# Kernel tuning notes

Hardware: AMD Instinct MI355X
Metric: run time of the kernel (lower is better)

The kernel has to match this reference:

```python
import jax, jax.numpy as jnp
import numpy as np

B, N, D = 4, 8192, 512
L, W, S = 64, 64, 32  # num_tokens, win_size, stride


def setup_inputs() -> dict:
    key = jax.random.key(0)
    ks = jax.random.split(key, 12)
    inp = {
        "feats": jax.random.normal(ks[0], (B, N, D), jnp.float32),
        "coords": jax.random.normal(ks[1], (B, N, 2), jnp.float32) * 100.0,
        "mask": jnp.zeros((B, N), dtype=bool),
        "z": jax.random.normal(ks[2], (L, D), jnp.float32) * 0.02,
        "Wq": jax.random.normal(ks[3], (D, D), jnp.float32) * 0.01,
        "Wk": jax.random.normal(ks[4], (D, D), jnp.float32) * 0.01,
        "Wv": jax.random.normal(ks[5], (D, D), jnp.float32) * 0.01,
        "W1": jax.random.normal(ks[6], (D, 2), jnp.float32) * 0.05,
        "b1": jnp.zeros((D,), jnp.float32),
        "W2": jax.random.normal(ks[7], (D, D), jnp.float32) * 0.01,
        "b2": jnp.zeros((D,), jnp.float32),
        "Wo": jax.random.normal(ks[8], (D, D), jnp.float32) * 0.01,
        "bo": jnp.zeros((D,), jnp.float32),
    }
    return inp


def reference(feats, coords, mask, z, Wq, Wk, Wv, W1, b1, W2, b2, Wo, bo):
    # mask is all-False: every token valid, N_valid == N, segments are
    # contiguous blocks of P = N // L tokens (seg_id = floor(i*L/N)).
    Bz, Nn, Dd = feats.shape
    Ll = z.shape[0]
    P = Nn // Ll  # tokens per segment

    # LayerNorm over feature dim (no affine, eps=1e-5 as in F.layer_norm)
    mu = feats.mean(-1, keepdims=True)
    var = feats.var(-1, keepdims=True)
    f_ln = (feats - mu) * jax.lax.rsqrt(var + 1e-5)

    # per-sample coordinate normalization (torch std is unbiased, ddof=1)
    c_mu = coords.mean(1, keepdims=True)
    c_sd = coords.std(1, keepdims=True, ddof=1) + 1e-8
    c_n = (coords - c_mu) / c_sd

    f_seg = f_ln.reshape(Bz, Ll, P, Dd)
    c_seg = c_n.reshape(Bz, Ll, P, 2)

    # static sliding windows within each segment (last window may be partial)
    starts = np.arange(0, P, S)                      # [nw]
    idx = starts[:, None] + np.arange(W)[None, :]    # [nw, W]
    valid = jnp.asarray(idx < P)                     # [nw, W] bool
    idx_c = np.minimum(idx, P - 1)
    cnt = valid.sum(-1).astype(feats.dtype)          # [nw]

    f_win = f_seg[:, :, idx_c]                       # [B,L,nw,W,D]
    c_win = c_seg[:, :, idx_c]                       # [B,L,nw,W,2]

    vmask = valid.astype(feats.dtype)[None, None, :, :, None]
    c_mean = (c_win * vmask).sum(3) / cnt[None, None, :, None]   # [B,L,nw,2]
    pos_in = c_win - c_mean[:, :, :, None, :]
    h = jax.nn.relu(jnp.einsum('blnwc,dc->blnwd', pos_in, W1) + b1)
    pos_bias = jnp.einsum('blnwd,ed->blnwe', h, W2) + b2

    q = z @ Wq.T                                     # [L,D]
    k = jnp.einsum('blnwd,ed->blnwe', f_win, Wk) + pos_bias
    v = jnp.einsum('blnwd,ed->blnwe', f_win, Wv)

    temperature = jnp.sqrt(jnp.asarray(Dd, feats.dtype))
    logits = jnp.einsum('ld,blnwd->blnw', q, k) / temperature
    logits = jnp.clip(logits, -10.0, 10.0)
    logits = jnp.where(valid[None, None], logits, -jnp.inf)
    attn = jax.nn.softmax(logits, axis=-1)           # [B,L,nw,W]

    z_win = jnp.einsum('blnw,blnwd->blnd', attn, v)  # [B,L,nw,D]
    z_l = z_win.mean(2)                              # average over windows
    return z_l @ Wo.T + bo                           # [B,L,D]
```

## Files before the change

kernel.cpp:

```cpp
#include <hip/hip_runtime.h>

#define Bz 4
#define Nn 8192
#define Dd 512
#define Ll 64
#define Pp 128
#define Ww 64
#define Ss 32
#define NW 4

__global__ __launch_bounds__(256) void pre1(
    const float* __restrict__ coords, const float* __restrict__ b2,
    const float* __restrict__ Wq, const float* __restrict__ Wk,
    const float* __restrict__ W2,
    const float* __restrict__ Wv, const float* __restrict__ Wo,
    float* __restrict__ cstats,
    float* __restrict__ M1, float* __restrict__ M2,
    float* __restrict__ WvoT, float* __restrict__ vb8) {
    __shared__ float As[64][65];
    __shared__ float Bs[64][36];
    __shared__ float b2s[64];
    __shared__ double dred[16];
    int bid = blockIdx.x, tid = threadIdx.x;
    int wv = tid >> 6, lane = tid & 63;

    if (bid < 384) {
        int role = bid >> 7;
        int wb = bid & 127;
        int m0 = (wb >> 4) * 64;
        int n0 = (wb & 15) * 32;
        const float* Amat = (role == 2) ? Wv : Wq;
        const float* Bmat = (role == 0) ? Wk : (role == 1) ? W2 : Wo;
        float* Cmat = (role == 0) ? M1 : (role == 1) ? M2 : WvoT;
        int tx = tid & 31, ty = tid >> 5;
        float acc[8] = {0.f, 0.f, 0.f, 0.f, 0.f, 0.f, 0.f, 0.f};
        for (int k0 = 0; k0 < Dd; k0 += 64) {
            int r = tid >> 4, c4 = (tid & 15) * 4;
#pragma unroll
            for (int i = 0; i < 4; ++i) {
                int kk = r + 16 * i;
                float4 v = *(const float4*)&Amat[(size_t)(k0 + kk) * Dd + m0 + c4];
                As[c4 + 0][kk] = v.x; As[c4 + 1][kk] = v.y;
                As[c4 + 2][kk] = v.z; As[c4 + 3][kk] = v.w;
            }
            if (role == 2) {
#pragma unroll
                for (int i = 0; i < 2; ++i) {
                    int nn = r + 16 * i;
                    float4 v = *(const float4*)&Bmat[(size_t)(n0 + nn) * Dd + k0 + c4];
                    Bs[c4 + 0][nn] = v.x; Bs[c4 + 1][nn] = v.y;
                    Bs[c4 + 2][nn] = v.z; Bs[c4 + 3][nn] = v.w;
                }
            } else {
                int kr = tid >> 3, c8 = (tid & 7) * 4;
#pragma unroll
                for (int i = 0; i < 2; ++i) {
                    int kk = kr + 32 * i;
                    float4 v = *(const float4*)&Bmat[(size_t)(k0 + kk) * Dd + n0 + c8];
                    *(float4*)&Bs[kk][c8] = v;
                }
            }
            __syncthreads();
#pragma unroll 16
            for (int kk = 0; kk < 64; ++kk) {
                float bv = Bs[kk][tx];
#pragma unroll
                for (int i = 0; i < 8; ++i)
                    acc[i] = fmaf(As[ty + 8 * i][kk], bv, acc[i]);
            }
            __syncthreads();
        }
#pragma unroll
        for (int i = 0; i < 8; ++i)
            Cmat[(size_t)(m0 + ty + 8 * i) * Dd + n0 + tx] = acc[i];
    } else if (bid < 392) {
        int j = bid - 384;
        if (tid < 64) b2s[tid] = b2[j * 64 + tid];
        __syncthreads();
        float a0 = 0.f, a1 = 0.f;
#pragma unroll 4
        for (int ee = 0; ee < 64; ++ee) {
            int e = j * 64 + ee;
            float be = b2s[ee];
            a0 = fmaf(be, Wq[(size_t)e * Dd + tid], a0);
            a1 = fmaf(be, Wq[(size_t)e * Dd + tid + 256], a1);
        }
        vb8[j * Dd + tid] = a0;
        vb8[j * Dd + tid + 256] = a1;
    } else {
        int b = bid - 392;
        double sx = 0, sy = 0, sxx = 0, syy = 0;
        const float4* cp = (const float4*)(coords + (size_t)b * Nn * 2);
        for (int i = tid; i < Nn / 2; i += 256) {
            float4 v = cp[i];
            sx  += (double)v.x + (double)v.z;
            sy  += (double)v.y + (double)v.w;
            sxx += (double)v.x * v.x + (double)v.z * v.z;
            syy += (double)v.y * v.y + (double)v.w * v.w;
        }
        for (int o = 32; o > 0; o >>= 1) {
            sx  += __shfl_down(sx,  o); sy  += __shfl_down(sy,  o);
            sxx += __shfl_down(sxx, o); syy += __shfl_down(syy, o);
        }
        if (lane == 0) {
            dred[wv * 4 + 0] = sx;  dred[wv * 4 + 1] = sy;
            dred[wv * 4 + 2] = sxx; dred[wv * 4 + 3] = syy;
        }
        __syncthreads();
        if (tid == 0) {
            double tx = 0, ty = 0, txx = 0, tyy = 0;
            for (int i = 0; i < 4; ++i) {
                tx += dred[i * 4 + 0]; ty += dred[i * 4 + 1];
                txx += dred[i * 4 + 2]; tyy += dred[i * 4 + 3];
            }
            const double N = (double)Nn;
            double mux = tx / N, muy = ty / N;
            double vx = (txx - N * mux * mux) / (N - 1.0);
            double vy = (tyy - N * muy * muy) / (N - 1.0);
            cstats[b * 4 + 0] = (float)mux;
            cstats[b * 4 + 1] = (float)muy;
            cstats[b * 4 + 2] = (float)sqrt(vx) + 1e-8f;
            cstats[b * 4 + 3] = (float)sqrt(vy) + 1e-8f;
        }
    }
}

__global__ __launch_bounds__(256) void qkg_k(
    const float* __restrict__ z, const float* __restrict__ M1,
    const float* __restrict__ M2, const float* __restrict__ vb8,
    float* __restrict__ QK, float* __restrict__ G,
    float* __restrict__ sqk4, float* __restrict__ qb2) {
    __shared__ float zs[Dd];
    __shared__ float pq[8][128];
    __shared__ float pg[8][128];
    __shared__ float red[8];
    int bid = blockIdx.x, tid = threadIdx.x;
    int l = bid & 63, ch = bid >> 6;
    int wv = tid >> 6, lane = tid & 63;

    zs[tid]       = z[(size_t)l * Dd + tid];
    zs[tid + 256] = z[(size_t)l * Dd + tid + 256];
    __syncthreads();

    if (ch == 0) {
        float vba = 0.f, vbb = 0.f;
#pragma unroll
        for (int j = 0; j < 8; ++j) {
            vba += vb8[j * Dd + tid];
            vbb += vb8[j * Dd + tid + 256];
        }
        float p = zs[tid] * vba + zs[tid + 256] * vbb;
        for (int o = 32; o > 0; o >>= 1) p += __shfl_xor(p, o);
        if (lane == 0) red[4 + wv] = p;
    }

    {
        int qd = tid & 31, h = tid >> 5;
        int cb = ch * 128 + qd * 4;
        float4 aq = make_float4(0.f, 0.f, 0.f, 0.f);
        float4 ag = make_float4(0.f, 0.f, 0.f, 0.f);
        for (int d = h * 64; d < h * 64 + 64; ++d) {
            float zd = zs[d];
            float4 m1 = *(const float4*)&M1[(size_t)d * Dd + cb];
            float4 m2 = *(const float4*)&M2[(size_t)d * Dd + cb];
            aq.x = fmaf(zd, m1.x, aq.x); aq.y = fmaf(zd, m1.y, aq.y);
            aq.z = fmaf(zd, m1.z, aq.z); aq.w = fmaf(zd, m1.w, aq.w);
            ag.x = fmaf(zd, m2.x, ag.x); ag.y = fmaf(zd, m2.y, ag.y);
            ag.z = fmaf(zd, m2.z, ag.z); ag.w = fmaf(zd, m2.w, ag.w);
        }
        *(float4*)&pq[h][qd * 4] = aq;
        *(float4*)&pg[h][qd * 4] = ag;
    }
    __syncthreads();
    if (tid < 128) {
        float vq = 0.f, vg = 0.f;
#pragma unroll
        for (int hh = 0; hh < 8; ++hh) { vq += pq[hh][tid]; vg += pg[hh][tid]; }
        QK[(size_t)l * Dd + ch * 128 + tid] = vq;
        G [(size_t)l * Dd + ch * 128 + tid] = vg;
        float s = vq;
        for (int o = 32; o > 0; o >>= 1) s += __shfl_xor(s, o);
        if (lane == 0) red[wv] = s;
    }
    __syncthreads();
    if (tid == 0) sqk4[ch * 64 + l] = red[0] + red[1];
    if (ch == 0 && tid == 32) qb2[l] = red[4] + red[5] + red[6] + red[7];
}

__global__ __launch_bounds__(512) void attn2(
    const float* __restrict__ feats, const float* __restrict__ coords,
    const float* __restrict__ cstats,
    const float* __restrict__ QKm, const float* __restrict__ Gm,
    const float* __restrict__ sqk4, const float* __restrict__ qb2,
    const float* __restrict__ W1, const float* __restrict__ b1,
    const float* __restrict__ WvoT, const float* __restrict__ bo,
    float* __restrict__ out) {
    __shared__ float  qk_s[Dd];
    __shared__ float4 wpack[Dd];
    __shared__ float  scx[Pp], scy[Pp];
    __shared__ float  smu[Pp], srs[Pp], sa[Pp];
    __shared__ float  shs[NW * Ww];
    __shared__ float  sar[NW][Ww];
    __shared__ float  swt[Pp];
    __shared__ float  scm[8];
    __shared__ float  s2red[NW];
    __shared__ float  soff;
    __shared__ float  red8[8][Dd];
    __shared__ float  fm_s[Dd];

    int bx = blockIdx.x;
    int l = bx & 63, b = bx >> 6;
    int tid = threadIdx.x;
    int wv = tid >> 6, lane = tid & 63;

    const float* fbase = feats + (size_t)bx * Pp * Dd;
    float4 f0[16], f1[16];
#pragma unroll
    for (int i = 0; i < 16; ++i) {
        const float4* fr = (const float4*)(fbase + (size_t)(wv * 16 + i) * Dd);
        f0[i] = fr[lane * 2];
        f1[i] = fr[lane * 2 + 1];
    }

    qk_s[tid]  = QKm[l * Dd + tid];
    wpack[tid] = make_float4(W1[2 * tid], W1[2 * tid + 1], b1[tid], Gm[l * Dd + tid]);
    if (tid < Pp) {
        int row = bx * Pp + tid;
        float x = coords[(size_t)row * 2], y = coords[(size_t)row * 2 + 1];
        scx[tid] = (x - cstats[b * 4 + 0]) / cstats[b * 4 + 2];
        scy[tid] = (y - cstats[b * 4 + 1]) / cstats[b * 4 + 3];
    }
    float sqk_l = sqk4[l] + sqk4[64 + l] + sqk4[128 + l] + sqk4[192 + l];
    float qb2_l = qb2[l];
    __syncthreads();

    if (wv < 4) {
        int n = wv, w = lane;
        int nv = (n == 3) ? 32 : 64;
        float cx = (w < nv) ? scx[n * Ss + w] : 0.f;
        float cy = (w < nv) ? scy[n * Ss + w] : 0.f;
        for (int o = 32; o > 0; o >>= 1) { cx += __shfl_xor(cx, o); cy += __shfl_xor(cy, o); }
        if (lane == 0) { scm[n] = cx / (float)nv; scm[4 + n] = cy / (float)nv; }
    }

    float4 q0 = ((const float4*)qk_s)[lane * 2];
    float4 q1 = ((const float4*)qk_s)[lane * 2 + 1];
    float sP[16], ssP[16], aP[16];
#pragma unroll
    for (int i = 0; i < 16; ++i) {
        float4 v0 = f0[i], v1 = f1[i];
        sP[i]  = v0.x + v0.y + v0.z + v0.w + v1.x + v1.y + v1.z + v1.w;
        ssP[i] = v0.x * v0.x + v0.y * v0.y + v0.z * v0.z + v0.w * v0.w
               + v1.x * v1.x + v1.y * v1.y + v1.z * v1.z + v1.w * v1.w;
        aP[i]  = v0.x * q0.x + v0.y * q0.y + v0.z * q0.z + v0.w * q0.w
               + v1.x * q1.x + v1.y * q1.y + v1.z * q1.z + v1.w * q1.w;
    }
#pragma unroll
    for (int i = 0; i < 16; ++i) {
        float s = sP[i], ss = ssP[i], a = aP[i];
        for (int o = 32; o > 0; o >>= 1) {
            s += __shfl_xor(s, o); ss += __shfl_xor(ss, o); a += __shfl_xor(a, o);
        }
        if (lane == 0) {
            int r = wv * 16 + i;
            float mu  = s * (1.f / (float)Dd);
            float var = ss * (1.f / (float)Dd) - mu * mu;
            smu[r] = mu; srs[r] = 1.f / sqrtf(var + 1e-5f); sa[r] = a;
        }
    }
    __syncthreads();

    {
        int s = tid >> 1, half = tid & 1;
        int n = s >> 6, w = s & 63;
        int nv = (n == 3) ? 32 : 64;
        float hs = 0.f;
        if (w < nv) {
            int p = n * Ss + w;
            float px = scx[p] - scm[n], py = scy[p] - scm[4 + n];
            int d0 = half * 256;
#pragma unroll 4
            for (int d = d0; d < d0 + 256; ++d) {
                float4 c = wpack[d];
                hs = fmaf(c.w, fmaxf(fmaf(c.x, px, fmaf(c.y, py, c.z)), 0.f), hs);
            }
        }
        hs += __shfl_xor(hs, 1);
        if (half == 0) shs[s] = hs;
    }
    __syncthreads();

    const float invtemp = 0.04419417382415922f;
    if (wv < 4) {
        int n = wv, w = lane;
        int nv = (n == 3) ? 32 : 64;
        int p = n * Ss + ((w < nv) ? w : 0);
        float lg = -1e30f;
        if (w < nv) {
            lg = (srs[p] * (sa[p] - smu[p] * sqk_l) + shs[n * Ww + w] + qb2_l) * invtemp;
            lg = fminf(fmaxf(lg, -10.f), 10.f);
        }
        float m = lg;
        for (int o = 32; o > 0; o >>= 1) m = fmaxf(m, __shfl_xor(m, o));
        float e = (w < nv) ? expf(lg - m) : 0.f;
        float ssum = e;
        for (int o = 32; o > 0; o >>= 1) ssum += __shfl_xor(ssum, o);
        float ar = (w < nv) ? (e / ssum) * srs[p] : 0.f;
        sar[n][w] = ar;
        float t2 = (w < nv) ? ar * smu[p] : 0.f;
        for (int o = 32; o > 0; o >>= 1) t2 += __shfl_xor(t2, o);
        if (lane == 0) s2red[n] = t2;
    }
    __syncthreads();

    if (tid < Pp) {
        int p = tid;
        int na = (p >> 5) - 1, nb = (p >> 5);
        float wt = 0.f;
        if (na >= 0 && na <= 3) wt += sar[na][p - na * Ss];
        if (nb <= 3)            wt += sar[nb][p - nb * Ss];
        swt[p] = wt;
    }
    if (tid == 0) soff = 0.25f * (s2red[0] + s2red[1] + s2red[2] + s2red[3]);
    __syncthreads();

    {
        float4 a0 = make_float4(0.f, 0.f, 0.f, 0.f);
        float4 a1 = make_float4(0.f, 0.f, 0.f, 0.f);
#pragma unroll
        for (int i = 0; i < 16; ++i) {
            float wt = swt[wv * 16 + i];
            a0.x = fmaf(wt, f0[i].x, a0.x); a0.y = fmaf(wt, f0[i].y, a0.y);
            a0.z = fmaf(wt, f0[i].z, a0.z); a0.w = fmaf(wt, f0[i].w, a0.w);
            a1.x = fmaf(wt, f1[i].x, a1.x); a1.y = fmaf(wt, f1[i].y, a1.y);
            a1.z = fmaf(wt, f1[i].z, a1.z); a1.w = fmaf(wt, f1[i].w, a1.w);
        }
        *(float4*)&red8[wv][lane * 8]     = a0;
        *(float4*)&red8[wv][lane * 8 + 4] = a1;
    }
    __syncthreads();
    {
        float v = 0.f;
#pragma unroll
        for (int w = 0; w < 8; ++w) v += red8[w][tid];
        fm_s[tid] = 0.25f * v - soff;
    }
    __syncthreads();

    {
        int cq = (tid & 127) * 4, h = tid >> 7;
        float4 acc = make_float4(0.f, 0.f, 0.f, 0.f);
#pragma unroll 4
        for (int e = h * 128; e < h * 128 + 128; ++e) {
            float fe = fm_s[e];
            float4 w = *(const float4*)&WvoT[(size_t)e * Dd + cq];
            acc.x = fmaf(fe, w.x, acc.x);
            acc.y = fmaf(fe, w.y, acc.y);
            acc.z = fmaf(fe, w.z, acc.z);
            acc.w = fmaf(fe, w.w, acc.w);
        }
        *(float4*)&red8[h][cq] = acc;
    }
    __syncthreads();
    out[(size_t)bx * Dd + tid] = bo[tid]
        + red8[0][tid] + red8[1][tid] + red8[2][tid] + red8[3][tid];
}

extern "C" void kernel_launch(void* const* d_in, const int* in_sizes, int n_in,
                              void* d_out, int out_size, void* d_ws, size_t ws_size,
                              hipStream_t stream) {
    const float* feats  = (const float*)d_in[0];
    const float* coords = (const float*)d_in[1];
    const float* z  = (const float*)d_in[3];
    const float* Wq = (const float*)d_in[4];
    const float* Wk = (const float*)d_in[5];
    const float* Wv = (const float*)d_in[6];
    const float* W1 = (const float*)d_in[7];
    const float* b1 = (const float*)d_in[8];
    const float* W2 = (const float*)d_in[9];
    const float* b2 = (const float*)d_in[10];
    const float* Wo = (const float*)d_in[11];
    const float* bo = (const float*)d_in[12];
    float* out = (float*)d_out;

    float* ws = (float*)d_ws;
    float* cstats = ws;
    float* M1     = ws + 16;
    float* M2     = M1 + Dd * Dd;
    float* WvoT   = M2 + Dd * Dd;
    float* vb8    = WvoT + Dd * Dd;
    float* QK     = vb8 + 8 * Dd;
    float* G      = QK + Ll * Dd;
    float* sqk4   = G + Ll * Dd;
    float* qb2    = sqk4 + 256;

    pre1<<<396, 256, 0, stream>>>(coords, b2, Wq, Wk, W2, Wv, Wo,
                                  cstats, M1, M2, WvoT, vb8);
    qkg_k<<<256, 256, 0, stream>>>(z, M1, M2, vb8, QK, G, sqk4, qb2);
    attn2<<<Bz * Ll, 512, 0, stream>>>(feats, coords, cstats,
                                       QK, G, sqk4, qb2, W1, b1,
                                       WvoT, bo, out);
}
```

Measured before the change: 199.6 us.

## Double attn2 block to 1024 threads and retile pre1 GEMMs to 4x4 outer products

The pre-GEMM kernel moves to 64x64 tiles, with each thread computing a 4x4 outer product from float4 shared-memory reads. This halves the block count and raises arithmetic per shared-memory load. The attention kernel grows from 512 to 1024 threads and holds 8 feature rows per wave in registers instead of 16, which cuts register pressure. The weighted row sum now re-reads feats from global memory instead of reusing registers. The aim is more latency hiding and parallelism in the memory-bound attention kernel, at the cost of a second pass over the feature data.

```diff
diff --git a/kernel.cpp b/kernel.cpp
--- a/kernel.cpp
+++ b/kernel.cpp
@@ -17,64 +17,74 @@
     float* __restrict__ cstats,
     float* __restrict__ M1, float* __restrict__ M2,
     float* __restrict__ WvoT, float* __restrict__ vb8) {
-    __shared__ float As[64][65];
-    __shared__ float Bs[64][36];
+    __shared__ float As[64][68];
+    __shared__ float Bs[64][68];
     __shared__ float b2s[64];
     __shared__ double dred[16];
     int bid = blockIdx.x, tid = threadIdx.x;
     int wv = tid >> 6, lane = tid & 63;
 
-    if (bid < 384) {
-        int role = bid >> 7;
-        int wb = bid & 127;
-        int m0 = (wb >> 4) * 64;
-        int n0 = (wb & 15) * 32;
+    if (bid < 192) {
+        int role = bid >> 6;
+        int wb = bid & 63;
+        int m0 = (wb >> 3) * 64;
+        int n0 = (wb & 7) * 64;
         const float* Amat = (role == 2) ? Wv : Wq;
         const float* Bmat = (role == 0) ? Wk : (role == 1) ? W2 : Wo;
         float* Cmat = (role == 0) ? M1 : (role == 1) ? M2 : WvoT;
-        int tx = tid & 31, ty = tid >> 5;
-        float acc[8] = {0.f, 0.f, 0.f, 0.f, 0.f, 0.f, 0.f, 0.f};
+        int tx = tid & 15, ty = tid >> 4;
+        float4 acc[4];
+#pragma unroll
+        for (int i = 0; i < 4; ++i) acc[i] = make_float4(0.f, 0.f, 0.f, 0.f);
+
         for (int k0 = 0; k0 < Dd; k0 += 64) {
-            int r = tid >> 4, c4 = (tid & 15) * 4;
-#pragma unroll
-            for (int i = 0; i < 4; ++i) {
-                int kk = r + 16 * i;
-                float4 v = *(const float4*)&Amat[(size_t)(k0 + kk) * Dd + m0 + c4];
-                As[c4 + 0][kk] = v.x; As[c4 + 1][kk] = v.y;
-                As[c4 + 2][kk] = v.z; As[c4 + 3][kk] = v.w;
-            }
-            if (role == 2) {
-#pragma unroll
-                for (int i = 0; i < 2; ++i) {
-                    int nn = r + 16 * i;
-                    float4 v = *(const float4*)&Bmat[(size_t)(n0 + nn) * Dd + k0 + c4];
-                    Bs[c4 + 0][nn] = v.x; Bs[c4 + 1][nn] = v.y;
-                    Bs[c4 + 2][nn] = v.z; Bs[c4 + 3][nn] = v.w;
+            {
+                int kk = tid >> 4, q4 = (tid & 15) * 4;
+#pragma unroll
+                for (int i = 0; i < 4; ++i) {
+                    int k = kk + 16 * i;
+                    *(float4*)&As[k][q4] =
+                        *(const float4*)&Amat[(size_t)(k0 + k) * Dd + m0 + q4];
                 }
-            } else {
-                int kr = tid >> 3, c8 = (tid & 7) * 4;
-#pragma unroll
-                for (int i = 0; i < 2; ++i) {
-                    int kk = kr + 32 * i;
-                    float4 v = *(const float4*)&Bmat[(size_t)(k0 + kk) * Dd + n0 + c8];
-                    *(float4*)&Bs[kk][c8] = v;
+                if (role != 2) {
+#pragma unroll
+                    for (int i = 0; i < 4; ++i) {
+                        int k = kk + 16 * i;
+                        *(float4*)&Bs[k][q4] =
+                            *(const float4*)&Bmat[(size_t)(k0 + k) * Dd + n0 + q4];
+                    }
+                } else {
+                    int d = tid >> 2;
+#pragma unroll
+                    for (int j = 0; j < 4; ++j) {
+                        int c0 = (tid & 3) * 16 + 4 * j;
+                        float4 v = *(const float4*)&Bmat[(size_t)(n0 + d) * Dd + k0 + c0];
+                        Bs[c0 + 0][d] = v.x; Bs[c0 + 1][d] = v.y;
+                        Bs[c0 + 2][d] = v.z; Bs[c0 + 3][d] = v.w;
+                    }
                 }
             }
             __syncthreads();
-#pragma unroll 16
+#pragma unroll 8
             for (int kk = 0; kk < 64; ++kk) {
-                float bv = Bs[kk][tx];
-#pragma unroll
-                for (int i = 0; i < 8; ++i)
-                    acc[i] = fmaf(As[ty + 8 * i][kk], bv, acc[i]);
+                float4 a4 = *(const float4*)&As[kk][ty * 4];
+                float4 b4 = *(const float4*)&Bs[kk][tx * 4];
+                acc[0].x = fmaf(a4.x, b4.x, acc[0].x); acc[0].y = fmaf(a4.x, b4.y, acc[0].y);
+                acc[0].z = fmaf(a4.x, b4.z, acc[0].z); acc[0].w = fmaf(a4.x, b4.w, acc[0].w);
+                acc[1].x = fmaf(a4.y, b4.x, acc[1].x); acc[1].y = fmaf(a4.y, b4.y, acc[1].y);
+                acc[1].z = fmaf(a4.y, b4.z, acc[1].z); acc[1].w = fmaf(a4.y, b4.w, acc[1].w);
+                acc[2].x = fmaf(a4.z, b4.x, acc[2].x); acc[2].y = fmaf(a4.z, b4.y, acc[2].y);
+                acc[2].z = fmaf(a4.z, b4.z, acc[2].z); acc[2].w = fmaf(a4.z, b4.w, acc[2].w);
+                acc[3].x = fmaf(a4.w, b4.x, acc[3].x); acc[3].y = fmaf(a4.w, b4.y, acc[3].y);
+                acc[3].z = fmaf(a4.w, b4.z, acc[3].z); acc[3].w = fmaf(a4.w, b4.w, acc[3].w);
             }
             __syncthreads();
         }
 #pragma unroll
-        for (int i = 0; i < 8; ++i)
-            Cmat[(size_t)(m0 + ty + 8 * i) * Dd + n0 + tx] = acc[i];
-    } else if (bid < 392) {
-        int j = bid - 384;
+        for (int i = 0; i < 4; ++i)
+            *(float4*)&Cmat[(size_t)(m0 + ty * 4 + i) * Dd + n0 + tx * 4] = acc[i];
+    } else if (bid < 200) {
+        int j = bid - 192;
         if (tid < 64) b2s[tid] = b2[j * 64 + tid];
         __syncthreads();
         float a0 = 0.f, a1 = 0.f;
@@ -88,7 +98,7 @@
         vb8[j * Dd + tid] = a0;
         vb8[j * Dd + tid + 256] = a1;
     } else {
-        int b = bid - 392;
+        int b = bid - 200;
         double sx = 0, sy = 0, sxx = 0, syy = 0;
         const float4* cp = (const float4*)(coords + (size_t)b * Nn * 2);
         for (int i = tid; i < Nn / 2; i += 256) {
@@ -187,7 +197,7 @@
     if (ch == 0 && tid == 32) qb2[l] = red[4] + red[5] + red[6] + red[7];
 }
 
-__global__ __launch_bounds__(512) void attn2(
+__global__ __launch_bounds__(1024) void attn2(
     const float* __restrict__ feats, const float* __restrict__ coords,
     const float* __restrict__ cstats,
     const float* __restrict__ QKm, const float* __restrict__ Gm,
@@ -206,7 +216,6 @@
     __shared__ float  s2red[NW];
     __shared__ float  soff;
     __shared__ float  red8[8][Dd];
-    __shared__ float  fm_s[Dd];
 
     int bx = blockIdx.x;
     int l = bx & 63, b = bx >> 6;
@@ -214,16 +223,25 @@
     int wv = tid >> 6, lane = tid & 63;
 
     const float* fbase = feats + (size_t)bx * Pp * Dd;
-    float4 f0[16], f1[16];
-#pragma unroll
-    for (int i = 0; i < 16; ++i) {
-        const float4* fr = (const float4*)(fbase + (size_t)(wv * 16 + i) * Dd);
-        f0[i] = fr[lane * 2];
-        f1[i] = fr[lane * 2 + 1];
-    }
-
-    qk_s[tid]  = QKm[l * Dd + tid];
-    wpack[tid] = make_float4(W1[2 * tid], W1[2 * tid + 1], b1[tid], Gm[l * Dd + tid]);
+    int rb = wv * 8;
+    float4 A0[4], A1[4], B0[4], B1[4];
+#pragma unroll
+    for (int i = 0; i < 4; ++i) {
+        const float4* fr = (const float4*)(fbase + (size_t)(rb + i) * Dd);
+        A0[i] = fr[lane * 2]; A1[i] = fr[lane * 2 + 1];
+    }
+#pragma unroll
+    for (int i = 0; i < 4; ++i) {
+        const float4* fr = (const float4*)(fbase + (size_t)(rb + 4 + i) * Dd);
+        B0[i] = fr[lane * 2]; B1[i] = fr[lane * 2 + 1];
+    }
+
+    if (tid < Dd) {
+        qk_s[tid] = QKm[l * Dd + tid];
+    } else {
+        int t = tid - Dd;
+        wpack[t] = make_float4(W1[2 * t], W1[2 * t + 1], b1[t], Gm[l * Dd + t]);
+    }
     if (tid < Pp) {
         int row = bx * Pp + tid;
         float x = coords[(size_t)row * 2], y = coords[(size_t)row * 2 + 1];
@@ -245,48 +263,81 @@
 
     float4 q0 = ((const float4*)qk_s)[lane * 2];
     float4 q1 = ((const float4*)qk_s)[lane * 2 + 1];
-    float sP[16], ssP[16], aP[16];
-#pragma unroll
-    for (int i = 0; i < 16; ++i) {
-        float4 v0 = f0[i], v1 = f1[i];
-        sP[i]  = v0.x + v0.y + v0.z + v0.w + v1.x + v1.y + v1.z + v1.w;
-        ssP[i] = v0.x * v0.x + v0.y * v0.y + v0.z * v0.z + v0.w * v0.w
-               + v1.x * v1.x + v1.y * v1.y + v1.z * v1.z + v1.w * v1.w;
-        aP[i]  = v0.x * q0.x + v0.y * q0.y + v0.z * q0.z + v0.w * q0.w
-               + v1.x * q1.x + v1.y * q1.y + v1.z * q1.z + v1.w * q1.w;
-    }
-#pragma unroll
-    for (int i = 0; i < 16; ++i) {
-        float s = sP[i], ss = ssP[i], a = aP[i];
+    {
+        float sP[4], ssP[4], aP[4];
+#pragma unroll
+        for (int i = 0; i < 4; ++i) {
+            float4 v0 = A0[i], v1 = A1[i];
+            sP[i]  = v0.x + v0.y + v0.z + v0.w + v1.x + v1.y + v1.z + v1.w;
+            ssP[i] = v0.x * v0.x + v0.y * v0.y + v0.z * v0.z + v0.w * v0.w
+                   + v1.x * v1.x + v1.y * v1.y + v1.z * v1.z + v1.w * v1.w;
+            aP[i]  = v0.x * q0.x + v0.y * q0.y + v0.z * q0.z + v0.w * q0.w
+                   + v1.x * q1.x + v1.y * q1.y + v1.z * q1.z + v1.w * q1.w;
+        }
+#pragma unroll
         for (int o = 32; o > 0; o >>= 1) {
-            s += __shfl_xor(s, o); ss += __shfl_xor(ss, o); a += __shfl_xor(a, o);
+#pragma unroll
+            for (int i = 0; i < 4; ++i) {
+                sP[i] += __shfl_xor(sP[i], o); ssP[i] += __shfl_xor(ssP[i], o);
+                aP[i] += __shfl_xor(aP[i], o);
+            }
         }
         if (lane == 0) {
-            int r = wv * 16 + i;
-            float mu  = s * (1.f / (float)Dd);
-            float var = ss * (1.f / (float)Dd) - mu * mu;
-            smu[r] = mu; srs[r] = 1.f / sqrtf(var + 1e-5f); sa[r] = a;
+#pragma unroll
+            for (int i = 0; i < 4; ++i) {
+                int r = rb + i;
+                float mu  = sP[i] * (1.f / (float)Dd);
+                float var = ssP[i] * (1.f / (float)Dd) - mu * mu;
+                smu[r] = mu; srs[r] = 1.f / sqrtf(var + 1e-5f); sa[r] = aP[i];
+            }
+        }
+#pragma unroll
+        for (int i = 0; i < 4; ++i) {
+            float4 v0 = B0[i], v1 = B1[i];
+            sP[i]  = v0.x + v0.y + v0.z + v0.w + v1.x + v1.y + v1.z + v1.w;
+            ssP[i] = v0.x * v0.x + v0.y * v0.y + v0.z * v0.z + v0.w * v0.w
+                   + v1.x * v1.x + v1.y * v1.y + v1.z * v1.z + v1.w * v1.w;
+            aP[i]  = v0.x * q0.x + v0.y * q0.y + v0.z * q0.z + v0.w * q0.w
+                   + v1.x * q1.x + v1.y * q1.y + v1.z * q1.z + v1.w * q1.w;
+        }
+#pragma unroll
+        for (int o = 32; o > 0; o >>= 1) {
+#pragma unroll
+            for (int i = 0; i < 4; ++i) {
+                sP[i] += __shfl_xor(sP[i], o); ssP[i] += __shfl_xor(ssP[i], o);
+                aP[i] += __shfl_xor(aP[i], o);
+            }
+        }
+        if (lane == 0) {
+#pragma unroll
+            for (int i = 0; i < 4; ++i) {
+                int r = rb + 4 + i;
+                float mu  = sP[i] * (1.f / (float)Dd);
+                float var = ssP[i] * (1.f / (float)Dd) - mu * mu;
+                smu[r] = mu; srs[r] = 1.f / sqrtf(var + 1e-5f); sa[r] = aP[i];
+            }
         }
     }
     __syncthreads();
 
     {
-        int s = tid >> 1, half = tid & 1;
+        int s = tid >> 2, q = tid & 3;
         int n = s >> 6, w = s & 63;
         int nv = (n == 3) ? 32 : 64;
         float hs = 0.f;
         if (w < nv) {
             int p = n * Ss + w;
             float px = scx[p] - scm[n], py = scy[p] - scm[4 + n];
-            int d0 = half * 256;
+            int d0 = q * 128;
 #pragma unroll 4
-            for (int d = d0; d < d0 + 256; ++d) {
+            for (int d = d0; d < d0 + 128; ++d) {
                 float4 c = wpack[d];
                 hs = fmaf(c.w, fmaxf(fmaf(c.x, px, fmaf(c.y, py, c.z)), 0.f), hs);
             }
         }
         hs += __shfl_xor(hs, 1);
-        if (half == 0) shs[s] = hs;
+        hs += __shfl_xor(hs, 2);
+        if (q == 0) shs[s] = hs;
     }
     __syncthreads();
 
@@ -325,34 +376,35 @@
     __syncthreads();
 
     {
-        float4 a0 = make_float4(0.f, 0.f, 0.f, 0.f);
-        float4 a1 = make_float4(0.f, 0.f, 0.f, 0.f);
-#pragma unroll
-        for (int i = 0; i < 16; ++i) {
-            float wt = swt[wv * 16 + i];
-            a0.x = fmaf(wt, f0[i].x, a0.x); a0.y = fmaf(wt, f0[i].y, a0.y);
-            a0.z = fmaf(wt, f0[i].z, a0.z); a0.w = fmaf(wt, f0[i].w, a0.w);
-            a1.x = fmaf(wt, f1[i].x, a1.x); a1.y = fmaf(wt, f1[i].y, a1.y);
-            a1.z = fmaf(wt, f1[i].z, a1.z); a1.w = fmaf(wt, f1[i].w, a1.w);
-        }
-        *(float4*)&red8[wv][lane * 8]     = a0;
-        *(float4*)&red8[wv][lane * 8 + 4] = a1;
-    }
-    __syncthreads();
-    {
-        float v = 0.f;
-#pragma unroll
-        for (int w = 0; w < 8; ++w) v += red8[w][tid];
-        fm_s[tid] = 0.25f * v - soff;
-    }
-    __syncthreads();
-
-    {
-        int cq = (tid & 127) * 4, h = tid >> 7;
+        int g = tid >> 7, c4 = tid & 127;
+        const float4* f4 = (const float4*)fbase;
         float4 acc = make_float4(0.f, 0.f, 0.f, 0.f);
 #pragma unroll 4
-        for (int e = h * 128; e < h * 128 + 128; ++e) {
-            float fe = fm_s[e];
+        for (int p = g; p < Pp; p += 8) {
+            float wt = swt[p];
+            float4 v = f4[p * 128 + c4];
+            acc.x = fmaf(wt, v.x, acc.x);
+            acc.y = fmaf(wt, v.y, acc.y);
+            acc.z = fmaf(wt, v.z, acc.z);
+            acc.w = fmaf(wt, v.w, acc.w);
+        }
+        *(float4*)&red8[g][c4 * 4] = acc;
+    }
+    __syncthreads();
+    if (tid < Dd) {
+        float v = 0.f;
+#pragma unroll
+        for (int w = 0; w < 8; ++w) v += red8[w][tid];
+        qk_s[tid] = 0.25f * v - soff;
+    }
+    __syncthreads();
+
+    {
+        int h = tid >> 7, cq = (tid & 127) * 4;
+        float4 acc = make_float4(0.f, 0.f, 0.f, 0.f);
+#pragma unroll 4
+        for (int e = h * 64; e < h * 64 + 64; ++e) {
+            float fe = qk_s[e];
             float4 w = *(const float4*)&WvoT[(size_t)e * Dd + cq];
             acc.x = fmaf(fe, w.x, acc.x);
             acc.y = fmaf(fe, w.y, acc.y);
@@ -362,8 +414,11 @@
         *(float4*)&red8[h][cq] = acc;
     }
     __syncthreads();
-    out[(size_t)bx * Dd + tid] = bo[tid]
-        + red8[0][tid] + red8[1][tid] + red8[2][tid] + red8[3][tid];
+    if (tid < Dd) {
+        out[(size_t)bx * Dd + tid] = bo[tid]
+            + red8[0][tid] + red8[1][tid] + red8[2][tid] + red8[3][tid]
+            + red8[4][tid] + red8[5][tid] + red8[6][tid] + red8[7][tid];
+    }
 }
 
 extern "C" void kernel_launch(void* const* d_in, const int* in_sizes, int n_in,
@@ -394,10 +449,10 @@
     float* sqk4   = G + Ll * Dd;
     float* qb2    = sqk4 + 256;
 
-    pre1<<<396, 256, 0, stream>>>(coords, b2, Wq, Wk, W2, Wv, Wo,
+    pre1<<<204, 256, 0, stream>>>(coords, b2, Wq, Wk, W2, Wv, Wo,
                                   cstats, M1, M2, WvoT, vb8);
     qkg_k<<<256, 256, 0, stream>>>(z, M1, M2, vb8, QK, G, sqk4, qb2);
-    attn2<<<Bz * Ll, 512, 0, stream>>>(feats, coords, cstats,
-                                       QK, G, sqk4, qb2, W1, b1,
-                                       WvoT, bo, out);
+    attn2<<<Bz * Ll, 1024, 0, stream>>>(feats, coords, cstats,
+                                        QK, G, sqk4, qb2, W1, b1,
+                                        WvoT, bo, out);
 }
```

Measured after the change: 187.1 us. -6.3%, faster.
